# Performance work log

Hardware: AMD Instinct MI355X
Metric: run time of the kernel (lower is better)

## Reference

```python
import jax, jax.numpy as jnp
from jax import lax
import numpy as np


def crf_log_likelihood(logits, tags, seqlen, trans):
    # logits [B,T,L], tags [B,T] int, seqlen [B] int, trans [L,L]
    B, T, L = logits.shape
    mask = jnp.arange(T)[None, :] < seqlen[:, None]  # [B,T] bool
    unary = jnp.take_along_axis(logits, tags[..., None], axis=2)[..., 0]  # [B,T]
    unary_score = jnp.sum(unary * mask, axis=1)
    binary = trans[tags[:, :-1], tags[:, 1:]]  # [B,T-1]
    binary_score = jnp.sum(binary * mask[:, 1:], axis=1)

    def step(alpha, inp):
        logit_t, m = inp  # [B,L], [B]
        new = jax.nn.logsumexp(alpha[:, :, None] + trans[None], axis=1) + logit_t
        return jnp.where(m[:, None], new, alpha), None

    xs = (jnp.moveaxis(logits[:, 1:], 1, 0), jnp.moveaxis(mask[:, 1:], 1, 0))
    alphaT, _ = lax.scan(step, logits[:, 0], xs)
    log_norm = jax.nn.logsumexp(alphaT, axis=1)  # [B]
    return unary_score + binary_score - log_norm


def crf_decode(logits, trans, seqlen):
    B, T, L = logits.shape
    mask = jnp.arange(T)[None, :] < seqlen[:, None]
    ident = jnp.broadcast_to(jnp.arange(L)[None, :], (B, L))

    def fwd(alpha, inp):
        logit_t, m = inp
        scores = alpha[:, :, None] + trans[None]  # [B,L,L]
        bp = jnp.argmax(scores, axis=1)  # [B,L] best prev tag for each cur tag
        new = jnp.max(scores, axis=1) + logit_t
        alpha = jnp.where(m[:, None], new, alpha)
        bp = jnp.where(m[:, None], bp, ident)  # identity bp on padded steps
        return alpha, bp

    xs = (jnp.moveaxis(logits[:, 1:], 1, 0), jnp.moveaxis(mask[:, 1:], 1, 0))
    alphaT, bps = lax.scan(fwd, logits[:, 0], xs)  # bps [T-1,B,L]
    last = jnp.argmax(alphaT, axis=1)  # [B]

    def back(tag, bp):
        prev = jnp.take_along_axis(bp, tag[:, None], axis=1)[:, 0]
        return prev, prev

    _, tags_prev = lax.scan(back, last, bps, reverse=True)  # [T-1,B]
    return jnp.concatenate([jnp.moveaxis(tags_prev, 1, 0), last[:, None]], axis=1)


def setup_inputs():
    key = jax.random.key(0)
    ks = jax.random.split(key, 8)
    B, T, D = 64, 512, 768
    L1, L2 = 2, 9
    x = jax.random.normal(ks[0], (B, T, D), dtype=jnp.float32)
    label = jax.random.randint(ks[1], (B, T), 0, L2)
    seqlen = jax.random.randint(ks[2], (B,), 1, T + 1)
    W1 = jax.random.truncated_normal(ks[3], -2.0, 2.0, (D, L1), jnp.float32) * 0.02
    b1 = jnp.zeros((L1,), jnp.float32)
    W2 = jax.random.truncated_normal(ks[4], -2.0, 2.0, (D, L2), jnp.float32) * 0.02
    b2 = jnp.zeros((L2,), jnp.float32)
    lim1 = float(np.sqrt(6.0 / (L1 + L1)))
    trans1 = jax.random.uniform(ks[5], (L1, L1), jnp.float32, -lim1, lim1)
    lim2 = float(np.sqrt(6.0 / (L2 + L2)))
    trans2 = jax.random.uniform(ks[6], (L2, L2), jnp.float32, -lim2, lim2)
    return {"x": x, "label": label, "seqlen": seqlen, "W1": W1, "b1": b1,
            "W2": W2, "b2": b2, "trans1": trans1, "trans2": trans2}


def reference(x, label, seqlen, W1, b1, W2, b2, trans1, trans2):
    T = x.shape[1]
    mask = (jnp.arange(T)[None, :] < seqlen[:, None]).astype(jnp.float32)
    total = jnp.sum(seqlen.astype(jnp.float32))

    label1 = jnp.where(label > 0, jnp.ones_like(label), jnp.zeros_like(label))
    out1 = x @ W1 + b1  # [B,T,2]
    ll1 = crf_log_likelihood(out1, label1, seqlen, trans1)
    loss1 = jnp.mean(-ll1)
    vit1 = crf_decode(out1, trans1, seqlen)
    acc1 = jnp.sum((vit1 == label1).astype(jnp.float32) * mask) / total

    out2 = x @ W2 + b2  # [B,T,9]
    ll2 = crf_log_likelihood(out2, label, seqlen, trans2)
    loss2 = jnp.mean(-ll2)
    vit2 = crf_decode(out2, trans2, seqlen)
    acc2 = jnp.sum((vit2 == label).astype(jnp.float32) * mask) / total

    loss = (loss1 + 8.0 * loss2) / 9.0
    viterbi = jnp.where(vit1 == 0, jnp.zeros_like(vit1), vit2)
    acc = jnp.sum((viterbi == label).astype(jnp.float32) * mask) / total
    return viterbi, loss, acc1, acc2, acc
```

## Files before the change

### kernel.cpp

```cpp
#include <hip/hip_runtime.h>

#define TT 512
#define BB 64
#define DD 768
#define NEG (-1e30f)

__device__ __forceinline__ float fmax3(float a, float b, float c) {
    return fmaxf(fmaxf(a, b), c);
}
__device__ __forceinline__ int imin3(int a, int b, int c) {
    return min(min(a, b), c);
}
__device__ __forceinline__ float rl(float x, int i) {
    return __int_as_float(__builtin_amdgcn_readlane(__float_as_int(x), i));
}
__device__ __forceinline__ float dot4(float4 a, float4 b) {
    return a.x * b.x + a.y * b.y + a.z * b.z + a.w * b.w;
}
__device__ __forceinline__ void gl_lds16(const float* g, float* l) {
    __builtin_amdgcn_global_load_lds(
        (const __attribute__((address_space(1))) void*)g,
        (__attribute__((address_space(3))) void*)l, 16, 0, 0);
}

__global__ __launch_bounds__(256) void gemm_kernel(
    const float* __restrict__ x,
    const float* __restrict__ W1, const float* __restrict__ b1,
    const float* __restrict__ W2, const float* __restrict__ b2,
    float* __restrict__ o1, float* __restrict__ o2)
{
    __shared__ float wT[11][DD];
    __shared__ float x_tile[2][128 * 64];

    const int tid = threadIdx.x;
    const int wave = tid >> 6, lane = tid & 63;

    for (int i = tid; i < 11 * DD; i += 256) {
        int m = i / DD, d = i - m * DD;
        wT[m][d] = (m < 2) ? W1[d * 2 + m] : W2[d * 9 + (m - 2)];
    }

    const int row0 = blockIdx.x * 128;
#define STAGE_TILE(KT, BF) { \
        _Pragma("unroll") \
        for (int i = 0; i < 8; ++i) { \
            const int e = i * 256 + tid; \
            const int r = e >> 4, q = e & 15; \
            const float* gp = x + ((size_t)(row0 + r) * DD + (KT) * 64 + q * 4); \
            gl_lds16(gp, &x_tile[BF][e * 4]); \
        } }

    STAGE_TILE(0, 0);
    __syncthreads();

    const int c = lane & 7, g = lane >> 3;
    const int rw = wave * 32 + g;

    float acc[4][11];
#pragma unroll
    for (int j = 0; j < 4; ++j)
#pragma unroll
        for (int m = 0; m < 11; ++m) acc[j][m] = 0.f;

    for (int kt = 0; kt < 12; ++kt) {
        const int cur = kt & 1;
        if (kt + 1 < 12) STAGE_TILE(kt + 1, cur ^ 1);

        float4 xr[4][2];
#pragma unroll
        for (int j = 0; j < 4; ++j) {
            const float* xp = &x_tile[cur][(rw + 8 * j) * 64 + c * 8];
            xr[j][0] = *(const float4*)(xp);
            xr[j][1] = *(const float4*)(xp + 4);
        }
#pragma unroll
        for (int m = 0; m < 11; ++m) {
            const float* wp = &wT[m][kt * 64 + c * 8];
            float4 wa = *(const float4*)(wp);
            float4 wb = *(const float4*)(wp + 4);
#pragma unroll
            for (int j = 0; j < 4; ++j)
                acc[j][m] += dot4(xr[j][0], wa) + dot4(xr[j][1], wb);
        }
        __syncthreads();
    }

#pragma unroll
    for (int j = 0; j < 4; ++j)
#pragma unroll
        for (int m = 0; m < 11; ++m) {
            acc[j][m] += __shfl_xor(acc[j][m], 1);
            acc[j][m] += __shfl_xor(acc[j][m], 2);
            acc[j][m] += __shfl_xor(acc[j][m], 4);
        }

    if (c == 0) {
        float bb1[2] = { b1[0], b1[1] };
        float bb2[9];
#pragma unroll
        for (int m = 0; m < 9; ++m) bb2[m] = b2[m];
#pragma unroll
        for (int j = 0; j < 4; ++j) {
            const int row = row0 + rw + 8 * j;
            o1[row * 2 + 0] = acc[j][0] + bb1[0];
            o1[row * 2 + 1] = acc[j][1] + bb1[1];
#pragma unroll
            for (int m = 0; m < 9; ++m) o2[row * 9 + m] = acc[j][m + 2] + bb2[m];
        }
    }
#undef STAGE_TILE
}

__global__ __launch_bounds__(256) void crf_kernel(
    const float* __restrict__ o1, const float* __restrict__ o2,
    const int* __restrict__ label, const int* __restrict__ seqlen,
    const float* __restrict__ trans1, const float* __restrict__ trans2,
    float* __restrict__ dout,
    float* __restrict__ M1, float* __restrict__ M2,
    float* __restrict__ scores, float* __restrict__ counts)
{
    __shared__ float s_l2[TT][9];
    __shared__ float s_l1[TT][2];
    __shared__ int   s_lab[TT];
    __shared__ float s_tr2[81];
    __shared__ float s_tr1[4];
    __shared__ __align__(8) unsigned char s_bp2[9][TT];
    __shared__ __align__(8) unsigned char s_bp1[2][TT];
    __shared__ unsigned char s_path2[16][9][36];
    __shared__ unsigned char s_path1[16][2][36];
    __shared__ unsigned char s_sel2[16], s_sel1[16];
    __shared__ float s_part[2][4];
    __shared__ int s_last2, s_last1;
    __shared__ int s_cnt[4][3];

    const int tid  = threadIdx.x;
    const int wave = tid >> 6, lane = tid & 63;

    if (blockIdx.x >= 64) {
        const int bc  = blockIdx.x - 64;
        const int b   = bc >> 4, cch = bc & 15;
        const int sl  = seqlen[b];
        const int t0  = cch * 32 + 1;
        const int cap = (cch < 15) ? 32 : 31;
        int n = sl - t0; n = n < 0 ? 0 : (n > cap ? cap : n);

        for (int i = tid; i < cap * 9; i += 256) {
            int t = i / 9, k = i - t * 9;
            s_l2[t][k] = o2[((size_t)b * TT + t0 + t) * 9 + k];
        }
        for (int i = tid; i < cap * 2; i += 256) {
            int t = i >> 1, k = i & 1;
            s_l1[t][k] = o1[((size_t)b * TT + t0 + t) * 2 + k];
        }
        if (tid < 81) s_tr2[tid] = trans2[tid];
        if (tid >= 128 && tid < 132) s_tr1[tid - 128] = trans1[tid - 128];
        __syncthreads();

        if (wave < 2) {
            int L, i_row, jj, base2; bool active;
            if (wave == 0) {
                if (lane < 63) { active = true;  L = 9; i_row = lane / 9; jj = lane - i_row * 9; base2 = i_row * 9; }
                else           { active = false; L = 9; i_row = 0; jj = 0; base2 = 54; }
            } else {
                if (lane < 18)      { active = true;  L = 9; i_row = 7 + lane / 9; jj = lane % 9; base2 = (lane / 9) * 9; }
                else if (lane < 22) { active = true;  L = 2; i_row = (lane - 18) >> 1; jj = (lane - 18) & 1; base2 = 18 + ((lane - 18) & ~1); }
                else                { active = false; L = 2; i_row = 0; jj = 0; base2 = 18; }
            }

            float tcol[9], row[9];
#pragma unroll
            for (int k = 0; k < 9; ++k) {
                tcol[k] = (k < L) ? ((L == 9) ? s_tr2[k * 9 + jj] : s_tr1[k * 2 + jj]) : NEG;
                row[k]  = (k < L && k == i_row) ? 0.f : NEG;
            }
            const float* lp = (L == 9) ? &s_l2[0][jj] : &s_l1[0][jj];
            const int lstride = L;

            for (int tt = 0; tt < n; ++tt) {
                float l = lp[tt * lstride];
                float v[9];
#pragma unroll
                for (int k = 0; k < 9; ++k) v[k] = row[k] + tcol[k];
                float m = fmax3(fmax3(v[0], v[1], v[2]), fmax3(v[3], v[4], v[5]), fmax3(v[6], v[7], v[8]));
                float s = 0.f;
#pragma unroll
                for (int k = 0; k < 9; ++k) s += __expf(v[k] - m);
                float nv = m + __logf(s) + l;
#pragma unroll
                for (int k = 0; k < 9; ++k) {
                    float sv = __shfl(nv, base2 + (k < L ? k : 0));
                    row[k] = (k < L) ? sv : NEG;
                }
            }
            if (active) {
                if (L == 9) M2[((size_t)(b * 16 + cch)) * 81 + i_row * 9 + jj] = row[jj];
                else        M1[((size_t)(b * 16 + cch)) * 4  + i_row * 2 + jj] = row[jj];
            }
        }
        return;
    }

    const int b  = blockIdx.x;
    const int sl = seqlen[b];

    {
        const float4* src = (const float4*)(o2 + (size_t)b * TT * 9);
        float4* dst = (float4*)&s_l2[0][0];
        for (int i = tid; i < TT * 9 / 4; i += 256) dst[i] = src[i];
    }
    {
        const float4* src = (const float4*)(o1 + (size_t)b * TT * 2);
        float4* dst = (float4*)&s_l1[0][0];
        for (int i = tid; i < TT * 2 / 4; i += 256) dst[i] = src[i];
    }
    {
        const int4* src = (const int4*)(label + (size_t)b * TT);
        int4* dst = (int4*)s_lab;
        for (int i = tid; i < TT / 4; i += 256) dst[i] = src[i];
    }
    if (tid < 81) s_tr2[tid] = trans2[tid];
    if (tid >= 96 && tid < 100) s_tr1[tid - 96] = trans1[tid - 96];
    for (int i = tid; i < 9 * TT; i += 256) ((unsigned char*)s_bp2)[i] = (unsigned char)(i >> 9);
    for (int i = tid; i < 2 * TT; i += 256) ((unsigned char*)s_bp1)[i] = (unsigned char)(i >> 9);
    __syncthreads();

    if (wave == 0) {
        if (lane < 9) {
            const int j = lane;
            float tc0 = s_tr2[0 * 9 + j], tc1 = s_tr2[1 * 9 + j], tc2 = s_tr2[2 * 9 + j];
            float tc3 = s_tr2[3 * 9 + j], tc4 = s_tr2[4 * 9 + j], tc5 = s_tr2[5 * 9 + j];
            float tc6 = s_tr2[6 * 9 + j], tc7 = s_tr2[7 * 9 + j], tc8 = s_tr2[8 * 9 + j];
            float av = s_l2[0][j];
            float a0 = rl(av, 0), a1 = rl(av, 1), a2 = rl(av, 2);
            float a3 = rl(av, 3), a4 = rl(av, 4), a5 = rl(av, 5);
            float a6 = rl(av, 6), a7 = rl(av, 7), a8 = rl(av, 8);

#define VSTEP2(LG, BI) { \
            float v0=a0+tc0, v1=a1+tc1, v2=a2+tc2, v3=a3+tc3, v4=a4+tc4; \
            float v5=a5+tc5, v6=a6+tc6, v7=a7+tc7, v8=a8+tc8; \
            float mm = fmax3(fmax3(v0,v1,v2), fmax3(v3,v4,v5), fmax3(v6,v7,v8)); \
            int c0=(v0==mm)?0:15, c1=(v1==mm)?1:15, c2=(v2==mm)?2:15; \
            int c3=(v3==mm)?3:15, c4=(v4==mm)?4:15, c5=(v5==mm)?5:15; \
            int c6=(v6==mm)?6:15, c7=(v7==mm)?7:15, c8=(v8==mm)?8:15; \
            BI = imin3(imin3(c0,c1,c2), imin3(c3,c4,c5), imin3(c6,c7,c8)); \
            float nj = mm + (LG); \
            a0=rl(nj,0); a1=rl(nj,1); a2=rl(nj,2); a3=rl(nj,3); a4=rl(nj,4); \
            a5=rl(nj,5); a6=rl(nj,6); a7=rl(nj,7); a8=rl(nj,8); }

            for (int t = 1; t < 8 && t < sl; ++t) {
                float lg = s_l2[t][j];
                int bi; VSTEP2(lg, bi);
                s_bp2[j][t] = (unsigned char)bi;
            }
            int t0 = 8;
            for (; t0 + 8 <= sl; t0 += 8) {
                float l0 = s_l2[t0 + 0][j], l1 = s_l2[t0 + 1][j];
                float l2 = s_l2[t0 + 2][j], l3 = s_l2[t0 + 3][j];
                float l4 = s_l2[t0 + 4][j], l5 = s_l2[t0 + 5][j];
                float l6 = s_l2[t0 + 6][j], l7 = s_l2[t0 + 7][j];
                int bi; unsigned int lo, hi;
                VSTEP2(l0, bi); lo  = (unsigned int)bi;
                VSTEP2(l1, bi); lo |= (unsigned int)bi << 8;
                VSTEP2(l2, bi); lo |= (unsigned int)bi << 16;
                VSTEP2(l3, bi); lo |= (unsigned int)bi << 24;
                VSTEP2(l4, bi); hi  = (unsigned int)bi;
                VSTEP2(l5, bi); hi |= (unsigned int)bi << 8;
                VSTEP2(l6, bi); hi |= (unsigned int)bi << 16;
                VSTEP2(l7, bi); hi |= (unsigned int)bi << 24;
                *(unsigned long long*)&s_bp2[j][t0] =
                    (unsigned long long)lo | ((unsigned long long)hi << 32);
            }
            for (int t = t0; t < sl; ++t) {
                float lg = s_l2[t][j];
                int bi; VSTEP2(lg, bi);
                s_bp2[j][t] = (unsigned char)bi;
            }
#undef VSTEP2
            if (lane == 0) {
                float mm = fmax3(fmax3(a0, a1, a2), fmax3(a3, a4, a5), fmax3(a6, a7, a8));
                int c0 = (a0 == mm) ? 0 : 15, c1 = (a1 == mm) ? 1 : 15, c2 = (a2 == mm) ? 2 : 15;
                int c3 = (a3 == mm) ? 3 : 15, c4 = (a4 == mm) ? 4 : 15, c5 = (a5 == mm) ? 5 : 15;
                int c6 = (a6 == mm) ? 6 : 15, c7 = (a7 == mm) ? 7 : 15, c8 = (a8 == mm) ? 8 : 15;
                s_last2 = imin3(imin3(c0, c1, c2), imin3(c3, c4, c5), imin3(c6, c7, c8));
            }
        }
    } else if (wave == 1) {
        if (lane < 2) {
            const int j = lane;
            float tc0 = s_tr1[0 * 2 + j], tc1 = s_tr1[1 * 2 + j];
            float av = s_l1[0][j];
            float a0 = rl(av, 0), a1 = rl(av, 1);

#define VSTEP1(LG, BI) { \
            float v0 = a0 + tc0, v1 = a1 + tc1; \
            BI = (v1 > v0) ? 1 : 0; \
            float nj = fmaxf(v0, v1) + (LG); \
            a0 = rl(nj, 0); a1 = rl(nj, 1); }

            for (int t = 1; t < 8 && t < sl; ++t) {
                float lg = s_l1[t][j];
                int bi; VSTEP1(lg, bi);
                s_bp1[j][t] = (unsigned char)bi;
            }
            int t0 = 8;
            for (; t0 + 8 <= sl; t0 += 8) {
                float l0 = s_l1[t0 + 0][j], l1 = s_l1[t0 + 1][j];
                float l2 = s_l1[t0 + 2][j], l3 = s_l1[t0 + 3][j];
                float l4 = s_l1[t0 + 4][j], l5 = s_l1[t0 + 5][j];
                float l6 = s_l1[t0 + 6][j], l7 = s_l1[t0 + 7][j];
                int bi; unsigned int lo, hi;
                VSTEP1(l0, bi); lo  = (unsigned int)bi;
                VSTEP1(l1, bi); lo |= (unsigned int)bi << 8;
                VSTEP1(l2, bi); lo |= (unsigned int)bi << 16;
                VSTEP1(l3, bi); lo |= (unsigned int)bi << 24;
                VSTEP1(l4, bi); hi  = (unsigned int)bi;
                VSTEP1(l5, bi); hi |= (unsigned int)bi << 8;
                VSTEP1(l6, bi); hi |= (unsigned int)bi << 16;
                VSTEP1(l7, bi); hi |= (unsigned int)bi << 24;
                *(unsigned long long*)&s_bp1[j][t0] =
                    (unsigned long long)lo | ((unsigned long long)hi << 32);
            }
            for (int t = t0; t < sl; ++t) {
                float lg = s_l1[t][j];
                int bi; VSTEP1(lg, bi);
                s_bp1[j][t] = (unsigned char)bi;
            }
#undef VSTEP1
            if (lane == 0) s_last1 = (a1 > a0) ? 1 : 0;
        }
    } else {
        const int t0i = tid - 128;
        float u1 = 0.f, bs1 = 0.f, u2 = 0.f, bs2 = 0.f;
        for (int t = t0i; t < sl; t += 128) {
            int lb = s_lab[t]; int lb1 = lb > 0 ? 1 : 0;
            u1 += s_l1[t][lb1];
            u2 += s_l2[t][lb];
            if (t >= 1) {
                int lp = s_lab[t - 1]; int lp1 = lp > 0 ? 1 : 0;
                bs1 += s_tr1[lp1 * 2 + lb1];
                bs2 += s_tr2[lp * 9 + lb];
            }
        }
        for (int off = 32; off; off >>= 1) {
            u1 += __shfl_down(u1, off); bs1 += __shfl_down(bs1, off);
            u2 += __shfl_down(u2, off); bs2 += __shfl_down(bs2, off);
        }
        if (lane == 0) {
            s_part[wave - 2][0] = u1; s_part[wave - 2][1] = bs1;
            s_part[wave - 2][2] = u2; s_part[wave - 2][3] = bs2;
        }
    }
    __syncthreads();

    if (tid < 144) {
        int cch = tid / 9, e = tid - cch * 9;
        int pe = (cch < 15) ? (cch + 1) * 32 : 511;
        int tag = e;
        for (int t = pe; t > cch * 32; --t) {
            tag = s_bp2[tag][t];
            s_path2[cch][e][t - 1 - cch * 32] = (unsigned char)tag;
        }
    } else if (tid >= 160 && tid < 192) {
        int k = tid - 160, cch = k >> 1, e = k & 1;
        int pe = (cch < 15) ? (cch + 1) * 32 : 511;
        int tag = e;
        for (int t = pe; t > cch * 32; --t) {
            tag = s_bp1[tag][t];
            s_path1[cch][e][t - 1 - cch * 32] = (unsigned char)tag;
        }
    } else if (tid >= 224 && tid < 228) {
        int k = tid - 224;
        scores[b * 4 + k] = s_part[0][k] + s_part[1][k];
    }
    __syncthreads();

    if (tid == 0) {
        int cur = s_last2;
        for (int c = 15; c >= 0; --c) { s_sel2[c] = (unsigned char)cur; cur = s_path2[c][cur][0]; }
    } else if (tid == 1) {
        int cur = s_last1;
        for (int c = 15; c >= 0; --c) { s_sel1[c] = (unsigned char)cur; cur = s_path1[c][cur][0]; }
    }
    __syncthreads();

    {
        int c1 = 0, c2 = 0, cc = 0;
        for (int p = tid; p < TT; p += 256) {
            int ch = p >> 5;
            int v2 = (p == 511) ? s_last2 : (int)s_path2[ch][s_sel2[ch]][p & 31];
            int v1 = (p == 511) ? s_last1 : (int)s_path1[ch][s_sel1[ch]][p & 31];
            int comb = (v1 == 0) ? 0 : v2;
            dout[(size_t)b * TT + p] = (float)comb;
            if (p < sl) {
                int lb = s_lab[p]; int lb1 = lb > 0 ? 1 : 0;
                c1 += (v1 == lb1); c2 += (v2 == lb); cc += (comb == lb);
            }
        }
        for (int off = 32; off; off >>= 1) {
            c1 += __shfl_down(c1, off); c2 += __shfl_down(c2, off); cc += __shfl_down(cc, off);
        }
        if (lane == 0) { s_cnt[wave][0] = c1; s_cnt[wave][1] = c2; s_cnt[wave][2] = cc; }
    }
    __syncthreads();
    if (tid == 0) {
        counts[b * 3 + 0] = (float)(s_cnt[0][0] + s_cnt[1][0] + s_cnt[2][0] + s_cnt[3][0]);
        counts[b * 3 + 1] = (float)(s_cnt[0][1] + s_cnt[1][1] + s_cnt[2][1] + s_cnt[3][1]);
        counts[b * 3 + 2] = (float)(s_cnt[0][2] + s_cnt[1][2] + s_cnt[2][2] + s_cnt[3][2]);
    }
}

__global__ __launch_bounds__(64) void finalize_kernel(
    const float* __restrict__ o1, const float* __restrict__ o2,
    const float* __restrict__ M1, const float* __restrict__ M2,
    const float* __restrict__ scores,
    float* __restrict__ ll1, float* __restrict__ ll2)
{
    __shared__ float sM2[16 * 81];
    __shared__ float sM1[16 * 4];
    const int s = blockIdx.x, lane = threadIdx.x;

    for (int i = lane; i < 16 * 81; i += 64) sM2[i] = M2[(size_t)s * 16 * 81 + i];
    for (int i = lane; i < 16 * 4;  i += 64) sM1[i] = M1[(size_t)s * 16 * 4 + i];
    __syncthreads();

    if (lane < 9) {
        const int r = lane;
        float av = o2[(size_t)s * TT * 9 + r];
        float a0 = rl(av, 0), a1 = rl(av, 1), a2 = rl(av, 2);
        float a3 = rl(av, 3), a4 = rl(av, 4), a5 = rl(av, 5);
        float a6 = rl(av, 6), a7 = rl(av, 7), a8 = rl(av, 8);
        for (int c = 0; c < 16; ++c) {
            const float* M = &sM2[c * 81];
            float v0 = a0 + M[0 * 9 + r], v1 = a1 + M[1 * 9 + r], v2 = a2 + M[2 * 9 + r];
            float v3 = a3 + M[3 * 9 + r], v4 = a4 + M[4 * 9 + r], v5 = a5 + M[5 * 9 + r];
            float v6 = a6 + M[6 * 9 + r], v7 = a7 + M[7 * 9 + r], v8 = a8 + M[8 * 9 + r];
            float m = fmax3(fmax3(v0, v1, v2), fmax3(v3, v4, v5), fmax3(v6, v7, v8));
            float su = __expf(v0 - m) + __expf(v1 - m) + __expf(v2 - m)
                     + __expf(v3 - m) + __expf(v4 - m) + __expf(v5 - m)
                     + __expf(v6 - m) + __expf(v7 - m) + __expf(v8 - m);
            float na = m + __logf(su);
            a0 = rl(na, 0); a1 = rl(na, 1); a2 = rl(na, 2);
            a3 = rl(na, 3); a4 = rl(na, 4); a5 = rl(na, 5);
            a6 = rl(na, 6); a7 = rl(na, 7); a8 = rl(na, 8);
        }
        if (lane == 0) {
            float m = fmax3(fmax3(a0, a1, a2), fmax3(a3, a4, a5), fmax3(a6, a7, a8));
            float su = __expf(a0 - m) + __expf(a1 - m) + __expf(a2 - m)
                     + __expf(a3 - m) + __expf(a4 - m) + __expf(a5 - m)
                     + __expf(a6 - m) + __expf(a7 - m) + __expf(a8 - m);
            float ln = m + __logf(su);
            ll2[s] = (scores[s * 4 + 2] + scores[s * 4 + 3]) - ln;
        }
    } else if (lane >= 16 && lane < 18) {
        const int jj = lane - 16;
        float av = o1[(size_t)s * TT * 2 + jj];
        float a0 = rl(av, 16), a1 = rl(av, 17);
        for (int c = 0; c < 16; ++c) {
            const float* M = &sM1[c * 4];
            float v0 = a0 + M[0 * 2 + jj], v1 = a1 + M[1 * 2 + jj];
            float mm = fmaxf(v0, v1);
            float na = mm + __logf(__expf(v0 - mm) + __expf(v1 - mm));
            a0 = rl(na, 16); a1 = rl(na, 17);
        }
        if (jj == 0) {
            float mm = fmaxf(a0, a1);
            float ln = mm + __logf(__expf(a0 - mm) + __expf(a1 - mm));
            ll1[s] = (scores[s * 4 + 0] + scores[s * 4 + 1]) - ln;
        }
    }
}

__global__ __launch_bounds__(64) void reduce_kernel(
    const float* __restrict__ ll1, const float* __restrict__ ll2,
    const float* __restrict__ counts, const int* __restrict__ seqlen,
    float* __restrict__ out)
{
    const int t = threadIdx.x;
    float v1 = ll1[t], v2 = ll2[t];
    float a1 = counts[t * 3 + 0], a2 = counts[t * 3 + 1], ac = counts[t * 3 + 2];
    float slf = (float)seqlen[t];
    for (int off = 32; off; off >>= 1) {
        v1 += __shfl_down(v1, off); v2 += __shfl_down(v2, off);
        a1 += __shfl_down(a1, off); a2 += __shfl_down(a2, off);
        ac += __shfl_down(ac, off); slf += __shfl_down(slf, off);
    }
    if (t == 0) {
        float loss1 = -v1 / 64.f;
        float loss2 = -v2 / 64.f;
        out[BB * TT + 0] = (loss1 + 8.f * loss2) / 9.f;
        out[BB * TT + 1] = a1 / slf;
        out[BB * TT + 2] = a2 / slf;
        out[BB * TT + 3] = ac / slf;
    }
}

extern "C" void kernel_launch(void* const* d_in, const int* in_sizes, int n_in,
                              void* d_out, int out_size, void* d_ws, size_t ws_size,
                              hipStream_t stream) {
    (void)in_sizes; (void)n_in; (void)out_size; (void)ws_size;
    const float* x      = (const float*)d_in[0];
    const int*   label  = (const int*)d_in[1];
    const int*   seqlen = (const int*)d_in[2];
    const float* W1     = (const float*)d_in[3];
    const float* b1     = (const float*)d_in[4];
    const float* W2     = (const float*)d_in[5];
    const float* b2     = (const float*)d_in[6];
    const float* trans1 = (const float*)d_in[7];
    const float* trans2 = (const float*)d_in[8];
    float* out = (float*)d_out;
    float* ws  = (float*)d_ws;

    float* o1     = ws;
    float* o2     = o1 + BB * TT * 2;
    float* M2     = o2 + BB * TT * 9;
    float* M1     = M2 + 64 * 16 * 81;
    float* scores = M1 + 64 * 16 * 4;
    float* counts = scores + 64 * 4;
    float* ll1    = counts + 64 * 3;
    float* ll2    = ll1 + BB;

    gemm_kernel<<<256, 256, 0, stream>>>(x, W1, b1, W2, b2, o1, o2);
    crf_kernel<<<1088, 256, 0, stream>>>(o1, o2, label, seqlen, trans1, trans2,
                                         out, M1, M2, scores, counts);
    finalize_kernel<<<64, 64, 0, stream>>>(o1, o2, M1, M2, scores, ll1, ll2);
    reduce_kernel<<<1, 64, 0, stream>>>(ll1, ll2, counts, seqlen, out);
}
```

Measured before the change: 239.4 us.

## Move Viterbi backpointer argmax off the serial recurrence into a parallel pass

The serial forward Viterbi loop now only computes the max recurrence and stores every alpha vector in shared memory. Backpointer argmax selection is recomputed afterwards from the stored alphas by all threads in parallel across time steps. This shortens the latency-bound critical chain of the single-wave recurrence, at the cost of extra LDS (about 22KB of alpha storage), an additional barrier and some redundant recomputation. The extra shared memory may reduce occupancy for the other blocks.

After: 222.3 us. -7.1%, faster.

```diff
diff --git a/kernel.cpp b/kernel.cpp
--- a/kernel.cpp
+++ b/kernel.cpp
@@ -121,11 +121,13 @@
 {
     __shared__ float s_l2[TT][9];
     __shared__ float s_l1[TT][2];
+    __shared__ float s_alpha2[TT][9];
+    __shared__ float s_alpha1[TT][2];
     __shared__ int   s_lab[TT];
     __shared__ float s_tr2[81];
     __shared__ float s_tr1[4];
-    __shared__ __align__(8) unsigned char s_bp2[9][TT];
-    __shared__ __align__(8) unsigned char s_bp1[2][TT];
+    __shared__ unsigned char s_bp2[9][TT];
+    __shared__ unsigned char s_bp1[2][TT];
     __shared__ unsigned char s_path2[16][9][36];
     __shared__ unsigned char s_path1[16][2][36];
     __shared__ unsigned char s_sel2[16], s_sel1[16];
@@ -231,26 +233,23 @@
             float tc3 = s_tr2[3 * 9 + j], tc4 = s_tr2[4 * 9 + j], tc5 = s_tr2[5 * 9 + j];
             float tc6 = s_tr2[6 * 9 + j], tc7 = s_tr2[7 * 9 + j], tc8 = s_tr2[8 * 9 + j];
             float av = s_l2[0][j];
+            s_alpha2[0][j] = av;
             float a0 = rl(av, 0), a1 = rl(av, 1), a2 = rl(av, 2);
             float a3 = rl(av, 3), a4 = rl(av, 4), a5 = rl(av, 5);
             float a6 = rl(av, 6), a7 = rl(av, 7), a8 = rl(av, 8);
 
-#define VSTEP2(LG, BI) { \
+#define VSTEP2(T, LG) { \
             float v0=a0+tc0, v1=a1+tc1, v2=a2+tc2, v3=a3+tc3, v4=a4+tc4; \
             float v5=a5+tc5, v6=a6+tc6, v7=a7+tc7, v8=a8+tc8; \
             float mm = fmax3(fmax3(v0,v1,v2), fmax3(v3,v4,v5), fmax3(v6,v7,v8)); \
-            int c0=(v0==mm)?0:15, c1=(v1==mm)?1:15, c2=(v2==mm)?2:15; \
-            int c3=(v3==mm)?3:15, c4=(v4==mm)?4:15, c5=(v5==mm)?5:15; \
-            int c6=(v6==mm)?6:15, c7=(v7==mm)?7:15, c8=(v8==mm)?8:15; \
-            BI = imin3(imin3(c0,c1,c2), imin3(c3,c4,c5), imin3(c6,c7,c8)); \
             float nj = mm + (LG); \
+            s_alpha2[T][j] = nj; \
             a0=rl(nj,0); a1=rl(nj,1); a2=rl(nj,2); a3=rl(nj,3); a4=rl(nj,4); \
             a5=rl(nj,5); a6=rl(nj,6); a7=rl(nj,7); a8=rl(nj,8); }
 
             for (int t = 1; t < 8 && t < sl; ++t) {
                 float lg = s_l2[t][j];
-                int bi; VSTEP2(lg, bi);
-                s_bp2[j][t] = (unsigned char)bi;
+                VSTEP2(t, lg);
             }
             int t0 = 8;
             for (; t0 + 8 <= sl; t0 += 8) {
@@ -258,22 +257,14 @@
                 float l2 = s_l2[t0 + 2][j], l3 = s_l2[t0 + 3][j];
                 float l4 = s_l2[t0 + 4][j], l5 = s_l2[t0 + 5][j];
                 float l6 = s_l2[t0 + 6][j], l7 = s_l2[t0 + 7][j];
-                int bi; unsigned int lo, hi;
-                VSTEP2(l0, bi); lo  = (unsigned int)bi;
-                VSTEP2(l1, bi); lo |= (unsigned int)bi << 8;
-                VSTEP2(l2, bi); lo |= (unsigned int)bi << 16;
-                VSTEP2(l3, bi); lo |= (unsigned int)bi << 24;
-                VSTEP2(l4, bi); hi  = (unsigned int)bi;
-                VSTEP2(l5, bi); hi |= (unsigned int)bi << 8;
-                VSTEP2(l6, bi); hi |= (unsigned int)bi << 16;
-                VSTEP2(l7, bi); hi |= (unsigned int)bi << 24;
-                *(unsigned long long*)&s_bp2[j][t0] =
-                    (unsigned long long)lo | ((unsigned long long)hi << 32);
+                VSTEP2(t0 + 0, l0); VSTEP2(t0 + 1, l1);
+                VSTEP2(t0 + 2, l2); VSTEP2(t0 + 3, l3);
+                VSTEP2(t0 + 4, l4); VSTEP2(t0 + 5, l5);
+                VSTEP2(t0 + 6, l6); VSTEP2(t0 + 7, l7);
             }
             for (int t = t0; t < sl; ++t) {
                 float lg = s_l2[t][j];
-                int bi; VSTEP2(lg, bi);
-                s_bp2[j][t] = (unsigned char)bi;
+                VSTEP2(t, lg);
             }
 #undef VSTEP2
             if (lane == 0) {
@@ -289,18 +280,18 @@
             const int j = lane;
             float tc0 = s_tr1[0 * 2 + j], tc1 = s_tr1[1 * 2 + j];
             float av = s_l1[0][j];
+            s_alpha1[0][j] = av;
             float a0 = rl(av, 0), a1 = rl(av, 1);
 
-#define VSTEP1(LG, BI) { \
+#define VSTEP1(T, LG) { \
             float v0 = a0 + tc0, v1 = a1 + tc1; \
-            BI = (v1 > v0) ? 1 : 0; \
             float nj = fmaxf(v0, v1) + (LG); \
+            s_alpha1[T][j] = nj; \
             a0 = rl(nj, 0); a1 = rl(nj, 1); }
 
             for (int t = 1; t < 8 && t < sl; ++t) {
                 float lg = s_l1[t][j];
-                int bi; VSTEP1(lg, bi);
-                s_bp1[j][t] = (unsigned char)bi;
+                VSTEP1(t, lg);
             }
             int t0 = 8;
             for (; t0 + 8 <= sl; t0 += 8) {
@@ -308,22 +299,14 @@
                 float l2 = s_l1[t0 + 2][j], l3 = s_l1[t0 + 3][j];
                 float l4 = s_l1[t0 + 4][j], l5 = s_l1[t0 + 5][j];
                 float l6 = s_l1[t0 + 6][j], l7 = s_l1[t0 + 7][j];
-                int bi; unsigned int lo, hi;
-                VSTEP1(l0, bi); lo  = (unsigned int)bi;
-                VSTEP1(l1, bi); lo |= (unsigned int)bi << 8;
-                VSTEP1(l2, bi); lo |= (unsigned int)bi << 16;
-                VSTEP1(l3, bi); lo |= (unsigned int)bi << 24;
-                VSTEP1(l4, bi); hi  = (unsigned int)bi;
-                VSTEP1(l5, bi); hi |= (unsigned int)bi << 8;
-                VSTEP1(l6, bi); hi |= (unsigned int)bi << 16;
-                VSTEP1(l7, bi); hi |= (unsigned int)bi << 24;
-                *(unsigned long long*)&s_bp1[j][t0] =
-                    (unsigned long long)lo | ((unsigned long long)hi << 32);
+                VSTEP1(t0 + 0, l0); VSTEP1(t0 + 1, l1);
+                VSTEP1(t0 + 2, l2); VSTEP1(t0 + 3, l3);
+                VSTEP1(t0 + 4, l4); VSTEP1(t0 + 5, l5);
+                VSTEP1(t0 + 6, l6); VSTEP1(t0 + 7, l7);
             }
             for (int t = t0; t < sl; ++t) {
                 float lg = s_l1[t][j];
-                int bi; VSTEP1(lg, bi);
-                s_bp1[j][t] = (unsigned char)bi;
+                VSTEP1(t, lg);
             }
 #undef VSTEP1
             if (lane == 0) s_last1 = (a1 > a0) ? 1 : 0;
@@ -348,6 +331,36 @@
         if (lane == 0) {
             s_part[wave - 2][0] = u1; s_part[wave - 2][1] = bs1;
             s_part[wave - 2][2] = u2; s_part[wave - 2][3] = bs2;
+        }
+    }
+    __syncthreads();
+
+    if (tid < 252) {
+        const int j = tid % 9;
+        const int tq = tid / 9;
+        float tc0 = s_tr2[0 * 9 + j], tc1 = s_tr2[1 * 9 + j], tc2 = s_tr2[2 * 9 + j];
+        float tc3 = s_tr2[3 * 9 + j], tc4 = s_tr2[4 * 9 + j], tc5 = s_tr2[5 * 9 + j];
+        float tc6 = s_tr2[6 * 9 + j], tc7 = s_tr2[7 * 9 + j], tc8 = s_tr2[8 * 9 + j];
+        for (int t = 1 + tq; t < sl; t += 28) {
+            const float* ap = &s_alpha2[t - 1][0];
+            float v0 = ap[0] + tc0, v1 = ap[1] + tc1, v2 = ap[2] + tc2;
+            float v3 = ap[3] + tc3, v4 = ap[4] + tc4, v5 = ap[5] + tc5;
+            float v6 = ap[6] + tc6, v7 = ap[7] + tc7, v8 = ap[8] + tc8;
+            float mm = fmax3(fmax3(v0, v1, v2), fmax3(v3, v4, v5), fmax3(v6, v7, v8));
+            int c0 = (v0 == mm) ? 0 : 15, c1 = (v1 == mm) ? 1 : 15, c2 = (v2 == mm) ? 2 : 15;
+            int c3 = (v3 == mm) ? 3 : 15, c4 = (v4 == mm) ? 4 : 15, c5 = (v5 == mm) ? 5 : 15;
+            int c6 = (v6 == mm) ? 6 : 15, c7 = (v7 == mm) ? 7 : 15, c8 = (v8 == mm) ? 8 : 15;
+            int bi = imin3(imin3(c0, c1, c2), imin3(c3, c4, c5), imin3(c6, c7, c8));
+            s_bp2[j][t] = (unsigned char)bi;
+        }
+    }
+    {
+        const int j1 = tid & 1;
+        float t10 = s_tr1[0 * 2 + j1], t11 = s_tr1[1 * 2 + j1];
+        for (int t = 1 + (tid >> 1); t < sl; t += 128) {
+            float v0 = s_alpha1[t - 1][0] + t10;
+            float v1 = s_alpha1[t - 1][1] + t11;
+            s_bp1[j1][t] = (unsigned char)((v1 > v0) ? 1 : 0);
         }
     }
     __syncthreads();
```
